# Kernel tuning notes

Measured on AMD Instinct MI355X. Metric: run time of the kernel, lower is better.

Reference implementation:

```python
import jax, jax.numpy as jnp
import numpy as np


def _reverse_padded(x, lengths):
    # x: [T, B, D]; reverse each sequence within its own length (packed-seq semantics)
    T = x.shape[0]
    t = jnp.arange(T)[:, None]                                   # [T, 1]
    idx = jnp.where(t < lengths[None, :], lengths[None, :] - 1 - t, t)  # [T, B]
    return jnp.take_along_axis(x, idx[:, :, None], axis=0)


def _lstm_dir(x, w_ih, w_hh, b):
    # single-direction LSTM, torch gate order (i, f, g, o). x: [T, B, Din]
    T, B, _ = x.shape
    H = w_hh.shape[1]
    xg = jnp.einsum('tbi,gi->tbg', x, w_ih) + b  # precompute input projections [T,B,4H]

    def step(carry, g_x):
        h, c = carry
        g = g_x + h @ w_hh.T
        i, f, gc, o = jnp.split(g, 4, axis=-1)
        c = jax.nn.sigmoid(f) * c + jax.nn.sigmoid(i) * jnp.tanh(gc)
        h = jax.nn.sigmoid(o) * jnp.tanh(c)
        return (h, c), h

    h0 = jnp.zeros((B, H), x.dtype)
    _, hs = jax.lax.scan(step, (h0, h0), xg)
    return hs  # [T, B, H]


def _bilstm_layer(x, lengths, wf, whf, bf, wr, whr, br):
    fwd = _lstm_dir(x, wf, whf, bf)
    rev = _reverse_padded(_lstm_dir(_reverse_padded(x, lengths), wr, whr, br), lengths)
    return jnp.concatenate([fwd, rev], axis=-1)  # [T, B, 2H]


def setup_inputs() -> dict:
    T, B, D, H = 256, 128, 300, 256
    key = jax.random.key(0)
    ks = jax.random.split(key, 24)
    stdv = 1.0 / np.sqrt(H)

    def u(k, shape):
        return jax.random.uniform(k, shape, jnp.float32, -stdv, stdv)

    inp = {
        'x': jax.random.normal(ks[0], (T, B, D), jnp.float32),
        'lengths': jax.random.randint(ks[1], (B,), 1, T + 1),
        # layer 0 forward / reverse
        'w_ih_l0': u(ks[2], (4 * H, D)), 'w_hh_l0': u(ks[3], (4 * H, H)),
        'b_ih_l0': u(ks[4], (4 * H,)), 'b_hh_l0': u(ks[5], (4 * H,)),
        'w_ih_l0r': u(ks[6], (4 * H, D)), 'w_hh_l0r': u(ks[7], (4 * H, H)),
        'b_ih_l0r': u(ks[8], (4 * H,)), 'b_hh_l0r': u(ks[9], (4 * H,)),
        # layer 1 forward / reverse (input dim 2H)
        'w_ih_l1': u(ks[10], (4 * H, 2 * H)), 'w_hh_l1': u(ks[11], (4 * H, H)),
        'b_ih_l1': u(ks[12], (4 * H,)), 'b_hh_l1': u(ks[13], (4 * H,)),
        'w_ih_l1r': u(ks[14], (4 * H, 2 * H)), 'w_hh_l1r': u(ks[15], (4 * H, H)),
        'b_ih_l1r': u(ks[16], (4 * H,)), 'b_hh_l1r': u(ks[17], (4 * H,)),
        # attention MLP + context vector
        'mlp_w': u(ks[18], (2 * H, 2 * H)),
        'mlp_b': u(ks[19], (2 * H,)),
        'ctx': jax.random.normal(ks[20], (2 * H,), jnp.float32) * 0.1,
    }
    return inp


def reference(x, lengths, w_ih_l0, w_hh_l0, b_ih_l0, b_hh_l0,
              w_ih_l0r, w_hh_l0r, b_ih_l0r, b_hh_l0r,
              w_ih_l1, w_hh_l1, b_ih_l1, b_hh_l1,
              w_ih_l1r, w_hh_l1r, b_ih_l1r, b_hh_l1r,
              mlp_w, mlp_b, ctx):
    lengths = jnp.maximum(lengths, 1)
    h1 = _bilstm_layer(x, lengths, w_ih_l0, w_hh_l0, b_ih_l0 + b_hh_l0,
                       w_ih_l0r, w_hh_l0r, b_ih_l0r + b_hh_l0r)
    h2 = _bilstm_layer(h1, lengths, w_ih_l1, w_hh_l1, b_ih_l1 + b_hh_l1,
                       w_ih_l1r, w_hh_l1r, b_ih_l1r + b_hh_l1r)
    out = h2.transpose(1, 0, 2)                                  # [B, T, 2H]
    ann = jnp.tanh(jnp.einsum('btd,ed->bte', out, mlp_w) + mlp_b)  # [B, T, 2H]
    scores = ann @ ctx                                           # [B, T]
    T = out.shape[1]
    mask = jnp.arange(T)[None, :] < lengths[:, None]             # [B, T]
    w = jax.nn.softmax(jnp.where(mask, scores, -1e9), axis=1)    # masked softmax over time
    return jnp.einsum('bt,btd->bd', w, out)                      # [B, 2H]
```

## Files before the change

kernel.cpp:

```cpp
#include <hip/hip_runtime.h>


#define T_ 256
#define B_ 128
#define D_ 300
#define H_ 256
#define G4H 1024
#define H2 512
#define TC 64
#define LDK 40
#define LDA 264

typedef __attribute__((ext_vector_type(8))) short bf16x8;
typedef __attribute__((ext_vector_type(4))) short short4v;
typedef __attribute__((ext_vector_type(4))) float f32x4;

#define MFMA16(a, b, c) __builtin_amdgcn_mfma_f32_16x16x32_bf16(a, b, c, 0, 0, 0)

__device__ __forceinline__ float sigf(float x) { return 1.f / (1.f + __expf(-x)); }
__device__ __forceinline__ float tanhfast(float x) { return 2.f / (1.f + __expf(-2.f * x)) - 1.f; }

__device__ __forceinline__ short hi_bf16(float x) {
  return (short)(__float_as_uint(x) >> 16);
}
__device__ __forceinline__ short lo_bf16(float x) {
  float lo = x - __uint_as_float(__float_as_uint(x) & 0xFFFF0000u);
  return (short)(__float_as_uint(lo) >> 16);
}

__device__ __forceinline__ void split_f4(const float4 v, short* hp, short* lp) {
  short4v h, l;
  h.x = hi_bf16(v.x); l.x = lo_bf16(v.x);
  h.y = hi_bf16(v.y); l.y = lo_bf16(v.y);
  h.z = hi_bf16(v.z); l.z = lo_bf16(v.z);
  h.w = hi_bf16(v.w); l.w = lo_bf16(v.w);
  *(short4v*)hp = h;
  *(short4v*)lp = l;
}

__device__ __forceinline__ void split8(const float4 v0, const float4 v1,
                                       bf16x8* hp, bf16x8* lp) {
  bf16x8 h, l;
  h[0] = hi_bf16(v0.x); l[0] = lo_bf16(v0.x);
  h[1] = hi_bf16(v0.y); l[1] = lo_bf16(v0.y);
  h[2] = hi_bf16(v0.z); l[2] = lo_bf16(v0.z);
  h[3] = hi_bf16(v0.w); l[3] = lo_bf16(v0.w);
  h[4] = hi_bf16(v1.x); l[4] = lo_bf16(v1.x);
  h[5] = hi_bf16(v1.y); l[5] = lo_bf16(v1.y);
  h[6] = hi_bf16(v1.z); l[6] = lo_bf16(v1.z);
  h[7] = hi_bf16(v1.w); l[7] = lo_bf16(v1.w);
  *hp = h; *lp = l;
}

__global__ __launch_bounds__(256, 2) void proj_gemm2(
    const float* __restrict__ X,
    const float* __restrict__ W0, const float* __restrict__ W1,
    const float* __restrict__ b1f, const float* __restrict__ b2f,
    const float* __restrict__ b1r, const float* __restrict__ b2r,
    float* __restrict__ C0, float* __restrict__ C1,
    int N, int K, const int* __restrict__ lengths, int t0)
{
  __shared__ short Xh[128 * LDK], Xl[128 * LDK];
  __shared__ short Wh[128 * LDK], Wl[128 * LDK];
  const int rev = blockIdx.z;
  const float* __restrict__ W = rev ? W1 : W0;
  const float* __restrict__ bias1 = rev ? b1r : b1f;
  const float* __restrict__ bias2 = rev ? b2r : b2f;
  float* __restrict__ C = rev ? C1 : C0;

  const int tid = threadIdx.x;
  const int m0 = blockIdx.y * 128, n0 = blockIdx.x * 128;
  const int s_step = t0 + blockIdx.y;

  const int sr = tid >> 3;
  const int sc = (tid & 7) * 4;
  const float* px[4];
  const float* pw[4];
#pragma unroll
  for (int p = 0; p < 4; p++) {
    const int r = sr + p * 32;
    int ss = s_step;
    if (rev) {
      int lb = lengths[r]; if (lb < 1) lb = 1;
      ss = (s_step < lb) ? (lb - 1 - s_step) : s_step;
    }
    px[p] = X + (size_t)(ss * 128 + r) * K;
    pw[p] = W + (size_t)(n0 + r) * K;
  }

  const int lane = tid & 63, w = tid >> 6;
  const int mb = (w & 1) * 64, nb = (w >> 1) * 64;
  const int r16 = lane & 15, quad = lane >> 4;

  f32x4 acc[4][4];
#pragma unroll
  for (int i = 0; i < 4; i++)
#pragma unroll
    for (int j = 0; j < 4; j++) acc[i][j] = (f32x4){0.f, 0.f, 0.f, 0.f};

  for (int k0 = 0; k0 < K; k0 += 32) {
    const int gk = k0 + sc;
    const bool kin = (gk < K);
#pragma unroll
    for (int p = 0; p < 4; p++) {
      float4 xv = {0.f, 0.f, 0.f, 0.f}, wv = {0.f, 0.f, 0.f, 0.f};
      if (kin) { xv = *(const float4*)(px[p] + gk); wv = *(const float4*)(pw[p] + gk); }
      const int ro = (sr + p * 32) * LDK + sc;
      split_f4(xv, &Xh[ro], &Xl[ro]);
      split_f4(wv, &Wh[ro], &Wl[ro]);
    }
    __syncthreads();

    bf16x8 ah[4], al[4], bh[4], bl[4];
#pragma unroll
    for (int mt = 0; mt < 4; mt++) {
      const int ro = (mb + mt * 16 + r16) * LDK + quad * 8;
      ah[mt] = *(const bf16x8*)&Xh[ro];
      al[mt] = *(const bf16x8*)&Xl[ro];
    }
#pragma unroll
    for (int nt = 0; nt < 4; nt++) {
      const int ro = (nb + nt * 16 + r16) * LDK + quad * 8;
      bh[nt] = *(const bf16x8*)&Wh[ro];
      bl[nt] = *(const bf16x8*)&Wl[ro];
    }
#pragma unroll
    for (int mt = 0; mt < 4; mt++)
#pragma unroll
      for (int nt = 0; nt < 4; nt++) {
        acc[mt][nt] = __builtin_amdgcn_mfma_f32_16x16x32_bf16(ah[mt], bh[nt], acc[mt][nt], 0, 0, 0);
        acc[mt][nt] = __builtin_amdgcn_mfma_f32_16x16x32_bf16(ah[mt], bl[nt], acc[mt][nt], 0, 0, 0);
        acc[mt][nt] = __builtin_amdgcn_mfma_f32_16x16x32_bf16(al[mt], bh[nt], acc[mt][nt], 0, 0, 0);
      }
    __syncthreads();
  }

  float bsum[4];
#pragma unroll
  for (int nt = 0; nt < 4; nt++) {
    const int col = n0 + nb + nt * 16 + r16;
    bsum[nt] = bias1[col] + bias2[col];
  }
#pragma unroll
  for (int mt = 0; mt < 4; mt++) {
    const int row = m0 + mb + mt * 16 + quad * 4;
#pragma unroll
    for (int nt = 0; nt < 4; nt++) {
      const int col = n0 + nb + nt * 16 + r16;
      float* Cp = C + (size_t)row * N + col;
#pragma unroll
      for (int reg = 0; reg < 4; reg++)
        Cp[(size_t)reg * N] = acc[mt][nt][reg] + bsum[nt];
    }
  }
}

__global__ __launch_bounds__(256, 2) void attn_gemm(
    const float* __restrict__ X, const float* __restrict__ W,
    const float* __restrict__ mlp_b, const float* __restrict__ ctx,
    float* __restrict__ scores, int M, int N, int K)
{
  __shared__ short Xh[128 * LDK], Xl[128 * LDK];
  __shared__ short Wh[128 * LDK], Wl[128 * LDK];
  const int tid = threadIdx.x;
  const int m0 = blockIdx.y * 128, n0 = blockIdx.x * 128;

  const int sr = tid >> 3;
  const int sc = (tid & 7) * 4;
  const float* px[4];
  const float* pw[4];
#pragma unroll
  for (int p = 0; p < 4; p++) {
    px[p] = X + (size_t)(m0 + sr + p * 32) * K;
    pw[p] = W + (size_t)(n0 + sr + p * 32) * K;
  }

  const int lane = tid & 63, w = tid >> 6;
  const int mb = (w & 1) * 64, nb = (w >> 1) * 64;
  const int r16 = lane & 15, quad = lane >> 4;

  f32x4 acc[4][4];
#pragma unroll
  for (int i = 0; i < 4; i++)
#pragma unroll
    for (int j = 0; j < 4; j++) acc[i][j] = (f32x4){0.f, 0.f, 0.f, 0.f};

  for (int k0 = 0; k0 < K; k0 += 32) {
    const int gk = k0 + sc;
#pragma unroll
    for (int p = 0; p < 4; p++) {
      float4 xv = *(const float4*)(px[p] + gk);
      float4 wv = *(const float4*)(pw[p] + gk);
      const int ro = (sr + p * 32) * LDK + sc;
      split_f4(xv, &Xh[ro], &Xl[ro]);
      split_f4(wv, &Wh[ro], &Wl[ro]);
    }
    __syncthreads();

    bf16x8 ah[4], al[4], bh[4], bl[4];
#pragma unroll
    for (int mt = 0; mt < 4; mt++) {
      const int ro = (mb + mt * 16 + r16) * LDK + quad * 8;
      ah[mt] = *(const bf16x8*)&Xh[ro];
      al[mt] = *(const bf16x8*)&Xl[ro];
    }
#pragma unroll
    for (int nt = 0; nt < 4; nt++) {
      const int ro = (nb + nt * 16 + r16) * LDK + quad * 8;
      bh[nt] = *(const bf16x8*)&Wh[ro];
      bl[nt] = *(const bf16x8*)&Wl[ro];
    }
#pragma unroll
    for (int mt = 0; mt < 4; mt++)
#pragma unroll
      for (int nt = 0; nt < 4; nt++) {
        acc[mt][nt] = __builtin_amdgcn_mfma_f32_16x16x32_bf16(ah[mt], bh[nt], acc[mt][nt], 0, 0, 0);
        acc[mt][nt] = __builtin_amdgcn_mfma_f32_16x16x32_bf16(ah[mt], bl[nt], acc[mt][nt], 0, 0, 0);
        acc[mt][nt] = __builtin_amdgcn_mfma_f32_16x16x32_bf16(al[mt], bh[nt], acc[mt][nt], 0, 0, 0);
      }
    __syncthreads();
  }

  float bb4[4], cc4[4];
#pragma unroll
  for (int nt = 0; nt < 4; nt++) {
    const int col = n0 + nb + nt * 16 + r16;
    bb4[nt] = mlp_b[col];
    cc4[nt] = ctx[col];
  }
#pragma unroll
  for (int mt = 0; mt < 4; mt++) {
#pragma unroll
    for (int reg = 0; reg < 4; reg++) {
      float ssum = 0.f;
#pragma unroll
      for (int nt = 0; nt < 4; nt++)
        ssum += tanhfast(acc[mt][nt][reg] + bb4[nt]) * cc4[nt];
      ssum += __shfl_xor(ssum, 1);
      ssum += __shfl_xor(ssum, 2);
      ssum += __shfl_xor(ssum, 4);
      ssum += __shfl_xor(ssum, 8);
      if (r16 == 0)
        atomicAdd(&scores[m0 + mb + mt * 16 + quad * 4 + reg], ssum);
    }
  }
}

__global__ __launch_bounds__(256, 1) void lstm_rec(
    const float* __restrict__ xgF, const float* __restrict__ xgR,
    const float* __restrict__ whF, const float* __restrict__ whR,
    const int* __restrict__ lengths, float* __restrict__ hout,
    float* __restrict__ ring, float* __restrict__ bbuf, float* __restrict__ cbuf,
    int t0)
{
  __shared__ short Ah[16 * LDA];
  __shared__ short Al[16 * LDA];
  __shared__ float gbuf[8 * 128];

  const int tid = threadIdx.x;
  const int blk = blockIdx.x;
  const int s = blk >> 5;
  const int d = (blk >> 4) & 1;
  const int g = blk & 15;
  const float* __restrict__ xg = d ? xgR : xgF;
  const float* __restrict__ wh = d ? whR : whF;

  const int lane = tid & 63;
  const int w = tid >> 6;
  const int r16 = lane & 15, quad = lane >> 4;

  const int cb = tid >> 5;
  const int hl = tid & 31;
  const int b = g * 8 + cb;
  const int hdim = s * 32 + hl;
  const int k0 = hl * 8;

  bf16x8 bh[2][8], bl[2][8];
#pragma unroll
  for (int nt = 0; nt < 2; nt++)
#pragma unroll
    for (int kt = 0; kt < 8; kt++) {
      const float* wr = wh + (size_t)(w * 256 + s * 32 + nt * 16 + r16) * 256
                           + kt * 32 + quad * 8;
      float4 v0 = *(const float4*)(wr);
      float4 v1 = *(const float4*)(wr + 4);
      split8(v0, v1, &bh[nt][kt], &bl[nt][kt]);
    }

  {
    int* za = (int*)(Ah + 8 * LDA);
    int* zb = (int*)(Al + 8 * LDA);
    for (int i = tid; i < (8 * LDA) / 2; i += 256) { za[i] = 0; zb[i] = 0; }
  }

  float c;
  if (t0 == 0) {
    int* za = (int*)Ah;
    int* zb = (int*)Al;
    for (int i = tid; i < (8 * LDA) / 2; i += 256) { za[i] = 0; zb[i] = 0; }
    c = 0.f;
  } else {
    const float* src = bbuf + ((size_t)d * 128 + g * 8 + cb) * 256 + k0;
    float4 v0 = *(const float4*)src;
    float4 v1 = *(const float4*)(src + 4);
    bf16x8 hv, lv;
    split8(v0, v1, &hv, &lv);
    *(bf16x8*)&Ah[cb * LDA + k0] = hv;
    *(bf16x8*)&Al[cb * LDA + k0] = lv;
    c = cbuf[((size_t)d * 128 + b) * 256 + hdim];
  }
  int lb = lengths[b]; if (lb < 1) lb = 1;

  const float* xr0 = xg + (size_t)b * 1024 + hdim;
  float x0 = xr0[0], x1 = xr0[256], x2 = xr0[512], x3 = xr0[768];
  __syncthreads();

  const int tend = t0 + TC;
  for (int t = t0; t < tend; t++) {
    const int slot = t - t0;
    const bool last = (t == tend - 1);

    f32x4 aH0 = {0.f,0.f,0.f,0.f}, aM0 = {0.f,0.f,0.f,0.f}, aL0 = {0.f,0.f,0.f,0.f};
    f32x4 aH1 = {0.f,0.f,0.f,0.f}, aM1 = {0.f,0.f,0.f,0.f}, aL1 = {0.f,0.f,0.f,0.f};
#pragma unroll
    for (int kt = 0; kt < 8; kt++) {
      const int ro = r16 * LDA + kt * 32 + quad * 8;
      bf16x8 ahf = *(const bf16x8*)&Ah[ro];
      bf16x8 alf = *(const bf16x8*)&Al[ro];
      aH0 = MFMA16(ahf, bh[0][kt], aH0);
      aM0 = MFMA16(ahf, bl[0][kt], aM0);
      aL0 = MFMA16(alf, bh[0][kt], aL0);
      aH1 = MFMA16(ahf, bh[1][kt], aH1);
      aM1 = MFMA16(ahf, bl[1][kt], aM1);
      aL1 = MFMA16(alf, bh[1][kt], aL1);
    }
    if (quad < 2) {
#pragma unroll
      for (int reg = 0; reg < 4; reg++) {
        gbuf[(quad * 4 + reg) * 128 + w * 32 + r16]      = aH0[reg] + aM0[reg] + aL0[reg];
        gbuf[(quad * 4 + reg) * 128 + w * 32 + 16 + r16] = aH1[reg] + aM1[reg] + aL1[reg];
      }
    }
    __syncthreads();

    const float gi = gbuf[cb * 128 +       hl] + x0;
    const float gf = gbuf[cb * 128 +  32 + hl] + x1;
    const float gg = gbuf[cb * 128 +  64 + hl] + x2;
    const float go = gbuf[cb * 128 +  96 + hl] + x3;
    const float si = sigf(gi), sf = sigf(gf);
    const float tg = tanhfast(gg), so = sigf(go);
    c = sf * c + si * tg;
    const float h = so * tanhfast(c);
    if (!last) {
      __hip_atomic_store(&ring[(((size_t)slot * 2 + d) * 128 + b) * 256 + hdim], h,
                         __ATOMIC_RELAXED, __HIP_MEMORY_SCOPE_AGENT);
    } else {
      bbuf[((size_t)d * 128 + b) * 256 + hdim] = h;
    }
    const int tin = d ? ((t < lb) ? (lb - 1 - t) : t) : t;
    hout[((size_t)tin * 128 + b) * 512 + d * 256 + hdim] = h;

    if (!last) {
      const float* xn = xg + ((size_t)(t + 1 - t0) * 128 + b) * 1024 + hdim;
      const float nx0 = xn[0], nx1 = xn[256], nx2 = xn[512], nx3 = xn[768];

      const unsigned* su = (const unsigned*)(ring +
          (((size_t)slot * 2 + d) * 128 + g * 8 + cb) * 256 + k0);
      unsigned uv[8];
      int it = 0;
      for (;;) {
        bool ok = true;
#pragma unroll
        for (int j = 0; j < 8; j++) {
          uv[j] = __hip_atomic_load(&su[j],
                                    __ATOMIC_RELAXED, __HIP_MEMORY_SCOPE_AGENT);
          ok &= (uv[j] != 0xFFFFFFFFu);
        }
        if (ok || ++it >= 20000) break;
      }
      float4 v0, v1;
      v0.x = __uint_as_float(uv[0]); v0.y = __uint_as_float(uv[1]);
      v0.z = __uint_as_float(uv[2]); v0.w = __uint_as_float(uv[3]);
      v1.x = __uint_as_float(uv[4]); v1.y = __uint_as_float(uv[5]);
      v1.z = __uint_as_float(uv[6]); v1.w = __uint_as_float(uv[7]);
      bf16x8 hv, lv;
      split8(v0, v1, &hv, &lv);
      *(bf16x8*)&Ah[cb * LDA + k0] = hv;
      *(bf16x8*)&Al[cb * LDA + k0] = lv;

      x0 = nx0; x1 = nx1; x2 = nx2; x3 = nx3;
      __syncthreads();
    }
  }
  cbuf[((size_t)d * 128 + b) * 256 + hdim] = c;
}

__global__ __launch_bounds__(256) void attn_final(
    const float* __restrict__ h2, const float* __restrict__ scores,
    const int* __restrict__ lengths, float* __restrict__ out)
{
  __shared__ float sl[256];
  __shared__ float red[256];
  const int b = blockIdx.x, tid = threadIdx.x;
  int lb = lengths[b]; if (lb < 1) lb = 1;
  const float sc = scores[(size_t)tid * 128 + b];
  const bool valid = (tid < lb);
  red[tid] = valid ? sc : -1e30f;
  __syncthreads();
  for (int off = 128; off > 0; off >>= 1) {
    if (tid < off) red[tid] = fmaxf(red[tid], red[tid + off]);
    __syncthreads();
  }
  const float mx = red[0];
  __syncthreads();
  const float p = valid ? __expf(sc - mx) : 0.f;
  red[tid] = p;
  __syncthreads();
  for (int off = 128; off > 0; off >>= 1) {
    if (tid < off) red[tid] += red[tid + off];
    __syncthreads();
  }
  const float inv = 1.f / red[0];
  __syncthreads();
  sl[tid] = p * inv;
  __syncthreads();

  float ax = 0.f, ay = 0.f;
  const int dd = tid * 2;
  for (int t = 0; t < 256; t++) {
    const float w = sl[t];
    if (w != 0.f) {
      const float* row = h2 + ((size_t)t * 128 + b) * 512 + dd;
      ax += w * row[0];
      ay += w * row[1];
    }
  }
  float2 r; r.x = ax; r.y = ay;
  *(float2*)(out + (size_t)b * 512 + dd) = r;
}

extern "C" void kernel_launch(void* const* d_in, const int* in_sizes, int n_in,
                              void* d_out, int out_size, void* d_ws, size_t ws_size,
                              hipStream_t stream) {
  (void)in_sizes; (void)n_in; (void)out_size; (void)ws_size;
  const float* x        = (const float*)d_in[0];
  const int*   lengths  = (const int*)d_in[1];
  const float* w_ih_l0  = (const float*)d_in[2];
  const float* w_hh_l0  = (const float*)d_in[3];
  const float* b_ih_l0  = (const float*)d_in[4];
  const float* b_hh_l0  = (const float*)d_in[5];
  const float* w_ih_l0r = (const float*)d_in[6];
  const float* w_hh_l0r = (const float*)d_in[7];
  const float* b_ih_l0r = (const float*)d_in[8];
  const float* b_hh_l0r = (const float*)d_in[9];
  const float* w_ih_l1  = (const float*)d_in[10];
  const float* w_hh_l1  = (const float*)d_in[11];
  const float* b_ih_l1  = (const float*)d_in[12];
  const float* b_hh_l1  = (const float*)d_in[13];
  const float* w_ih_l1r = (const float*)d_in[14];
  const float* w_hh_l1r = (const float*)d_in[15];
  const float* b_ih_l1r = (const float*)d_in[16];
  const float* b_hh_l1r = (const float*)d_in[17];
  const float* mlp_w    = (const float*)d_in[18];
  const float* mlp_b    = (const float*)d_in[19];
  const float* ctx      = (const float*)d_in[20];
  float* out = (float*)d_out;

  float* ws = (float*)d_ws;
  const size_t XGC    = (size_t)TC * B_ * G4H;
  const size_t H_SZ   = (size_t)T_ * B_ * H2;
  const size_t RINGSZ = (size_t)TC * 2 * B_ * H_;
  float* xgA    = ws;
  float* xgB    = xgA + XGC;
  float* h1     = xgB + XGC;
  float* h2     = h1 + H_SZ;
  float* ring   = h2 + H_SZ;
  float* bbuf   = ring + RINGSZ;
  float* cbuf   = bbuf + 65536;
  float* scores = cbuf + 65536;

  (void)hipMemsetAsync(scores, 0, 32768 * 4, stream);

  dim3 blk(256);
  const dim3 pgrid(G4H / 128, TC, 2);

  for (int c = 0; c < T_ / TC; c++) {
    const int t0 = c * TC;
    proj_gemm2<<<pgrid, blk, 0, stream>>>(x, w_ih_l0, w_ih_l0r,
                                          b_ih_l0, b_hh_l0, b_ih_l0r, b_hh_l0r,
                                          xgA, xgB, G4H, D_, lengths, t0);
    (void)hipMemsetAsync(ring, 0xFF, RINGSZ * 4, stream);
    lstm_rec<<<256, blk, 0, stream>>>(xgA, xgB, w_hh_l0, w_hh_l0r, lengths, h1,
                                      ring, bbuf, cbuf, t0);
  }
  for (int c = 0; c < T_ / TC; c++) {
    const int t0 = c * TC;
    proj_gemm2<<<pgrid, blk, 0, stream>>>(h1, w_ih_l1, w_ih_l1r,
                                          b_ih_l1, b_hh_l1, b_ih_l1r, b_hh_l1r,
                                          xgA, xgB, G4H, H2, lengths, t0);
    (void)hipMemsetAsync(ring, 0xFF, RINGSZ * 4, stream);
    lstm_rec<<<256, blk, 0, stream>>>(xgA, xgB, w_hh_l1, w_hh_l1r, lengths, h2,
                                      ring, bbuf, cbuf, t0);
  }
  attn_gemm<<<dim3(H2 / 128, (T_ * B_) / 128), blk, 0, stream>>>(h2, mlp_w, mlp_b, ctx, scores, T_ * B_, H2, H2);
  attn_final<<<B_, blk, 0, stream>>>(h2, scores, lengths, out);
}
```

Baseline: 2.385 ms.

## Process 32 batch rows per LSTM recurrence block and launch 64 blocks

The persistent recurrence kernel is regridded so each block handles 32 batch rows (two 16-row MFMA tiles) instead of 8, shrinking the grid from 256 to 64 blocks. Each block now does more MFMA work per step, but fewer blocks spin on the global ring buffer, and the same register-resident W_hh slices are reused across twice as many rows. The cost is fewer CUs in use and a longer serial critical path per timestep, since each block computes two tiles per step.

```diff
diff --git a/kernel.cpp b/kernel.cpp
--- a/kernel.cpp
+++ b/kernel.cpp
@@ -253,15 +253,16 @@
     float* __restrict__ ring, float* __restrict__ bbuf, float* __restrict__ cbuf,
     int t0)
 {
-  __shared__ short Ah[16 * LDA];
-  __shared__ short Al[16 * LDA];
-  __shared__ float gbuf[8 * 128];
+  __shared__ short Ah[2][16 * LDA];
+  __shared__ short Al[2][16 * LDA];
+  __shared__ float gbuf[2][16 * 128];
 
   const int tid = threadIdx.x;
   const int blk = blockIdx.x;
-  const int s = blk >> 5;
-  const int d = (blk >> 4) & 1;
-  const int g = blk & 15;
+  const int s = blk >> 3;
+  const int d = (blk >> 2) & 1;
+  const int p = blk & 3;
+  const int bbase = p * 32;
   const float* __restrict__ xg = d ? xgR : xgF;
   const float* __restrict__ wh = d ? whR : whF;
 
@@ -269,13 +270,13 @@
   const int w = tid >> 6;
   const int r16 = lane & 15, quad = lane >> 4;
 
-  const int cb = tid >> 5;
+  const int rb = tid >> 4;
+  const int kc = (tid & 15) * 16;
+  const int q = tid >> 5;
   const int hl = tid & 31;
-  const int b = g * 8 + cb;
   const int hdim = s * 32 + hl;
-  const int k0 = hl * 8;
-
-  bf16x8 bh[2][8], bl[2][8];
+
+  bf16x8 wbh[2][8], wbl[2][8];
 #pragma unroll
   for (int nt = 0; nt < 2; nt++)
 #pragma unroll
@@ -284,35 +285,52 @@
                            + kt * 32 + quad * 8;
       float4 v0 = *(const float4*)(wr);
       float4 v1 = *(const float4*)(wr + 4);
-      split8(v0, v1, &bh[nt][kt], &bl[nt][kt]);
-    }
-
-  {
-    int* za = (int*)(Ah + 8 * LDA);
-    int* zb = (int*)(Al + 8 * LDA);
-    for (int i = tid; i < (8 * LDA) / 2; i += 256) { za[i] = 0; zb[i] = 0; }
-  }
-
-  float c;
+      split8(v0, v1, &wbh[nt][kt], &wbl[nt][kt]);
+    }
+
+  float cc[2][2];
+  int   lbv[2][2];
+  float xreg[2][2][4];
+#pragma unroll
+  for (int u = 0; u < 2; u++)
+#pragma unroll
+    for (int hf = 0; hf < 2; hf++) {
+      const int b = bbase + u * 16 + hf * 8 + q;
+      int lb = lengths[b]; if (lb < 1) lb = 1;
+      lbv[u][hf] = lb;
+      const float* xr = xg + (size_t)b * 1024 + hdim;
+      xreg[u][hf][0] = xr[0];   xreg[u][hf][1] = xr[256];
+      xreg[u][hf][2] = xr[512]; xreg[u][hf][3] = xr[768];
+    }
+
   if (t0 == 0) {
-    int* za = (int*)Ah;
-    int* zb = (int*)Al;
-    for (int i = tid; i < (8 * LDA) / 2; i += 256) { za[i] = 0; zb[i] = 0; }
-    c = 0.f;
+    int* za = (int*)&Ah[0][0];
+    int* zb = (int*)&Al[0][0];
+    for (int i = tid; i < (2 * 16 * LDA) / 2; i += 256) { za[i] = 0; zb[i] = 0; }
+#pragma unroll
+    for (int u = 0; u < 2; u++)
+#pragma unroll
+      for (int hf = 0; hf < 2; hf++) cc[u][hf] = 0.f;
   } else {
-    const float* src = bbuf + ((size_t)d * 128 + g * 8 + cb) * 256 + k0;
-    float4 v0 = *(const float4*)src;
-    float4 v1 = *(const float4*)(src + 4);
-    bf16x8 hv, lv;
-    split8(v0, v1, &hv, &lv);
-    *(bf16x8*)&Ah[cb * LDA + k0] = hv;
-    *(bf16x8*)&Al[cb * LDA + k0] = lv;
-    c = cbuf[((size_t)d * 128 + b) * 256 + hdim];
-  }
-  int lb = lengths[b]; if (lb < 1) lb = 1;
-
-  const float* xr0 = xg + (size_t)b * 1024 + hdim;
-  float x0 = xr0[0], x1 = xr0[256], x2 = xr0[512], x3 = xr0[768];
+#pragma unroll
+    for (int u = 0; u < 2; u++) {
+      const float* src = bbuf + ((size_t)d * 128 + bbase + u * 16 + rb) * 256 + kc;
+      float4 v0 = *(const float4*)(src);
+      float4 v1 = *(const float4*)(src + 4);
+      float4 v2 = *(const float4*)(src + 8);
+      float4 v3 = *(const float4*)(src + 12);
+      bf16x8 hv, lv;
+      split8(v0, v1, &hv, &lv);
+      *(bf16x8*)&Ah[u][rb * LDA + kc] = hv;
+      *(bf16x8*)&Al[u][rb * LDA + kc] = lv;
+      split8(v2, v3, &hv, &lv);
+      *(bf16x8*)&Ah[u][rb * LDA + kc + 8] = hv;
+      *(bf16x8*)&Al[u][rb * LDA + kc + 8] = lv;
+#pragma unroll
+      for (int hf = 0; hf < 2; hf++)
+        cc[u][hf] = cbuf[((size_t)d * 128 + bbase + u * 16 + hf * 8 + q) * 256 + hdim];
+    }
+  }
   __syncthreads();
 
   const int tend = t0 + TC;
@@ -320,79 +338,108 @@
     const int slot = t - t0;
     const bool last = (t == tend - 1);
 
-    f32x4 aH0 = {0.f,0.f,0.f,0.f}, aM0 = {0.f,0.f,0.f,0.f}, aL0 = {0.f,0.f,0.f,0.f};
-    f32x4 aH1 = {0.f,0.f,0.f,0.f}, aM1 = {0.f,0.f,0.f,0.f}, aL1 = {0.f,0.f,0.f,0.f};
-#pragma unroll
-    for (int kt = 0; kt < 8; kt++) {
-      const int ro = r16 * LDA + kt * 32 + quad * 8;
-      bf16x8 ahf = *(const bf16x8*)&Ah[ro];
-      bf16x8 alf = *(const bf16x8*)&Al[ro];
-      aH0 = MFMA16(ahf, bh[0][kt], aH0);
-      aM0 = MFMA16(ahf, bl[0][kt], aM0);
-      aL0 = MFMA16(alf, bh[0][kt], aL0);
-      aH1 = MFMA16(ahf, bh[1][kt], aH1);
-      aM1 = MFMA16(ahf, bl[1][kt], aM1);
-      aL1 = MFMA16(alf, bh[1][kt], aL1);
-    }
-    if (quad < 2) {
+#pragma unroll
+    for (int u = 0; u < 2; u++) {
+      f32x4 aH0 = {0.f,0.f,0.f,0.f}, aM0 = {0.f,0.f,0.f,0.f}, aL0 = {0.f,0.f,0.f,0.f};
+      f32x4 aH1 = {0.f,0.f,0.f,0.f}, aM1 = {0.f,0.f,0.f,0.f}, aL1 = {0.f,0.f,0.f,0.f};
+#pragma unroll
+      for (int kt = 0; kt < 8; kt++) {
+        const int ro = r16 * LDA + kt * 32 + quad * 8;
+        bf16x8 ahf = *(const bf16x8*)&Ah[u][ro];
+        bf16x8 alf = *(const bf16x8*)&Al[u][ro];
+        aH0 = MFMA16(ahf, wbh[0][kt], aH0);
+        aM0 = MFMA16(ahf, wbl[0][kt], aM0);
+        aL0 = MFMA16(alf, wbh[0][kt], aL0);
+        aH1 = MFMA16(ahf, wbh[1][kt], aH1);
+        aM1 = MFMA16(ahf, wbl[1][kt], aM1);
+        aL1 = MFMA16(alf, wbh[1][kt], aL1);
+      }
 #pragma unroll
       for (int reg = 0; reg < 4; reg++) {
-        gbuf[(quad * 4 + reg) * 128 + w * 32 + r16]      = aH0[reg] + aM0[reg] + aL0[reg];
-        gbuf[(quad * 4 + reg) * 128 + w * 32 + 16 + r16] = aH1[reg] + aM1[reg] + aL1[reg];
+        gbuf[u][(quad * 4 + reg) * 128 + w * 32 + r16]      = aH0[reg] + aM0[reg] + aL0[reg];
+        gbuf[u][(quad * 4 + reg) * 128 + w * 32 + 16 + r16] = aH1[reg] + aM1[reg] + aL1[reg];
       }
     }
     __syncthreads();
 
-    const float gi = gbuf[cb * 128 +       hl] + x0;
-    const float gf = gbuf[cb * 128 +  32 + hl] + x1;
-    const float gg = gbuf[cb * 128 +  64 + hl] + x2;
-    const float go = gbuf[cb * 128 +  96 + hl] + x3;
-    const float si = sigf(gi), sf = sigf(gf);
-    const float tg = tanhfast(gg), so = sigf(go);
-    c = sf * c + si * tg;
-    const float h = so * tanhfast(c);
+#pragma unroll
+    for (int u = 0; u < 2; u++)
+#pragma unroll
+      for (int hf = 0; hf < 2; hf++) {
+        const int rbq = hf * 8 + q;
+        const int b = bbase + u * 16 + rbq;
+        const float gi = gbuf[u][rbq * 128 +       hl] + xreg[u][hf][0];
+        const float gf = gbuf[u][rbq * 128 +  32 + hl] + xreg[u][hf][1];
+        const float gg = gbuf[u][rbq * 128 +  64 + hl] + xreg[u][hf][2];
+        const float go = gbuf[u][rbq * 128 +  96 + hl] + xreg[u][hf][3];
+        const float si = sigf(gi), sf = sigf(gf);
+        const float tg = tanhfast(gg), so = sigf(go);
+        float c = sf * cc[u][hf] + si * tg;
+        cc[u][hf] = c;
+        const float h = so * tanhfast(c);
+        if (!last) {
+          __hip_atomic_store(&ring[(((size_t)slot * 2 + d) * 128 + b) * 256 + hdim], h,
+                             __ATOMIC_RELAXED, __HIP_MEMORY_SCOPE_AGENT);
+        } else {
+          bbuf[((size_t)d * 128 + b) * 256 + hdim] = h;
+        }
+        const int lb = lbv[u][hf];
+        const int tin = d ? ((t < lb) ? (lb - 1 - t) : t) : t;
+        hout[((size_t)tin * 128 + b) * 512 + d * 256 + hdim] = h;
+      }
+
     if (!last) {
-      __hip_atomic_store(&ring[(((size_t)slot * 2 + d) * 128 + b) * 256 + hdim], h,
-                         __ATOMIC_RELAXED, __HIP_MEMORY_SCOPE_AGENT);
-    } else {
-      bbuf[((size_t)d * 128 + b) * 256 + hdim] = h;
-    }
-    const int tin = d ? ((t < lb) ? (lb - 1 - t) : t) : t;
-    hout[((size_t)tin * 128 + b) * 512 + d * 256 + hdim] = h;
-
-    if (!last) {
-      const float* xn = xg + ((size_t)(t + 1 - t0) * 128 + b) * 1024 + hdim;
-      const float nx0 = xn[0], nx1 = xn[256], nx2 = xn[512], nx3 = xn[768];
-
-      const unsigned* su = (const unsigned*)(ring +
-          (((size_t)slot * 2 + d) * 128 + g * 8 + cb) * 256 + k0);
-      unsigned uv[8];
-      int it = 0;
-      for (;;) {
-        bool ok = true;
-#pragma unroll
-        for (int j = 0; j < 8; j++) {
-          uv[j] = __hip_atomic_load(&su[j],
-                                    __ATOMIC_RELAXED, __HIP_MEMORY_SCOPE_AGENT);
-          ok &= (uv[j] != 0xFFFFFFFFu);
+#pragma unroll
+      for (int u = 0; u < 2; u++)
+#pragma unroll
+        for (int hf = 0; hf < 2; hf++) {
+          const int b = bbase + u * 16 + hf * 8 + q;
+          const float* xn = xg + ((size_t)(t + 1 - t0) * 128 + b) * 1024 + hdim;
+          xreg[u][hf][0] = xn[0];   xreg[u][hf][1] = xn[256];
+          xreg[u][hf][2] = xn[512]; xreg[u][hf][3] = xn[768];
         }
-        if (ok || ++it >= 20000) break;
+
+#pragma unroll
+      for (int u = 0; u < 2; u++) {
+        const unsigned* su = (const unsigned*)(ring +
+            (((size_t)slot * 2 + d) * 128 + bbase + u * 16 + rb) * 256 + kc);
+        unsigned uv[16];
+        int it = 0;
+        for (;;) {
+          bool ok = true;
+#pragma unroll
+          for (int j = 0; j < 16; j++) {
+            uv[j] = __hip_atomic_load(&su[j],
+                                      __ATOMIC_RELAXED, __HIP_MEMORY_SCOPE_AGENT);
+            ok &= (uv[j] != 0xFFFFFFFFu);
+          }
+          if (ok || ++it >= 20000) break;
+        }
+        float4 v0, v1;
+        bf16x8 hv, lv;
+        v0.x = __uint_as_float(uv[0]);  v0.y = __uint_as_float(uv[1]);
+        v0.z = __uint_as_float(uv[2]);  v0.w = __uint_as_float(uv[3]);
+        v1.x = __uint_as_float(uv[4]);  v1.y = __uint_as_float(uv[5]);
+        v1.z = __uint_as_float(uv[6]);  v1.w = __uint_as_float(uv[7]);
+        split8(v0, v1, &hv, &lv);
+        *(bf16x8*)&Ah[u][rb * LDA + kc] = hv;
+        *(bf16x8*)&Al[u][rb * LDA + kc] = lv;
+        v0.x = __uint_as_float(uv[8]);  v0.y = __uint_as_float(uv[9]);
+        v0.z = __uint_as_float(uv[10]); v0.w = __uint_as_float(uv[11]);
+        v1.x = __uint_as_float(uv[12]); v1.y = __uint_as_float(uv[13]);
+        v1.z = __uint_as_float(uv[14]); v1.w = __uint_as_float(uv[15]);
+        split8(v0, v1, &hv, &lv);
+        *(bf16x8*)&Ah[u][rb * LDA + kc + 8] = hv;
+        *(bf16x8*)&Al[u][rb * LDA + kc + 8] = lv;
       }
-      float4 v0, v1;
-      v0.x = __uint_as_float(uv[0]); v0.y = __uint_as_float(uv[1]);
-      v0.z = __uint_as_float(uv[2]); v0.w = __uint_as_float(uv[3]);
-      v1.x = __uint_as_float(uv[4]); v1.y = __uint_as_float(uv[5]);
-      v1.z = __uint_as_float(uv[6]); v1.w = __uint_as_float(uv[7]);
-      bf16x8 hv, lv;
-      split8(v0, v1, &hv, &lv);
-      *(bf16x8*)&Ah[cb * LDA + k0] = hv;
-      *(bf16x8*)&Al[cb * LDA + k0] = lv;
-
-      x0 = nx0; x1 = nx1; x2 = nx2; x3 = nx3;
       __syncthreads();
     }
   }
-  cbuf[((size_t)d * 128 + b) * 256 + hdim] = c;
+#pragma unroll
+  for (int u = 0; u < 2; u++)
+#pragma unroll
+    for (int hf = 0; hf < 2; hf++)
+      cbuf[((size_t)d * 128 + bbase + u * 16 + hf * 8 + q) * 256 + hdim] = cc[u][hf];
 }
 
 __global__ __launch_bounds__(256) void attn_final(
@@ -490,8 +537,8 @@
                                           b_ih_l0, b_hh_l0, b_ih_l0r, b_hh_l0r,
                                           xgA, xgB, G4H, D_, lengths, t0);
     (void)hipMemsetAsync(ring, 0xFF, RINGSZ * 4, stream);
-    lstm_rec<<<256, blk, 0, stream>>>(xgA, xgB, w_hh_l0, w_hh_l0r, lengths, h1,
-                                      ring, bbuf, cbuf, t0);
+    lstm_rec<<<64, blk, 0, stream>>>(xgA, xgB, w_hh_l0, w_hh_l0r, lengths, h1,
+                                     ring, bbuf, cbuf, t0);
   }
   for (int c = 0; c < T_ / TC; c++) {
     const int t0 = c * TC;
@@ -499,8 +546,8 @@
                                           b_ih_l1, b_hh_l1, b_ih_l1r, b_hh_l1r,
                                           xgA, xgB, G4H, H2, lengths, t0);
     (void)hipMemsetAsync(ring, 0xFF, RINGSZ * 4, stream);
-    lstm_rec<<<256, blk, 0, stream>>>(xgA, xgB, w_hh_l1, w_hh_l1r, lengths, h2,
-                                      ring, bbuf, cbuf, t0);
+    lstm_rec<<<64, blk, 0, stream>>>(xgA, xgB, w_hh_l1, w_hh_l1r, lengths, h2,
+                                     ring, bbuf, cbuf, t0);
   }
   attn_gemm<<<dim3(H2 / 128, (T_ * B_) / 128), blk, 0, stream>>>(h2, mlp_w, mlp_b, ctx, scores, T_ * B_, H2, H2);
   attn_final<<<B_, blk, 0, stream>>>(h2, scores, lengths, out);
```

Measured after the change: 4.114 ms. 72.4% more time.

## Interleave both LSTM directions per block with 16-row batch tiles and bf16 ring exchange

Applied to the files above, without the earlier changes.

The recurrent kernel drops from 256 to 64 blocks. Each block now holds weights for both directions and processes 16 batch rows instead of 8, so the full 16-row MFMA tile is used rather than half of it being zero padding. The two directions alternate inside each time step, so one direction's spin-wait on the cross-block ring can overlap the other's compute. The ring now carries pre-split bf16 hi/lo halves packed in 32-bit words, which removes the split work on the consumer side. In exchange, register pressure roughly doubles from holding two weight sets, and each block has more work per step on the serial chain.

```diff
diff --git a/kernel.cpp b/kernel.cpp
--- a/kernel.cpp
+++ b/kernel.cpp
@@ -16,6 +16,8 @@
 typedef __attribute__((ext_vector_type(4))) float f32x4;
 
 #define MFMA16(a, b, c) __builtin_amdgcn_mfma_f32_16x16x32_bf16(a, b, c, 0, 0, 0)
+#define ATOM_ST(p, v) __hip_atomic_store((p), (v), __ATOMIC_RELAXED, __HIP_MEMORY_SCOPE_AGENT)
+#define ATOM_LD(p) __hip_atomic_load((p), __ATOMIC_RELAXED, __HIP_MEMORY_SCOPE_AGENT)
 
 __device__ __forceinline__ float sigf(float x) { return 1.f / (1.f + __expf(-x)); }
 __device__ __forceinline__ float tanhfast(float x) { return 2.f / (1.f + __expf(-2.f * x)) - 1.f; }
@@ -253,146 +255,184 @@
     float* __restrict__ ring, float* __restrict__ bbuf, float* __restrict__ cbuf,
     int t0)
 {
-  __shared__ short Ah[16 * LDA];
-  __shared__ short Al[16 * LDA];
-  __shared__ float gbuf[8 * 128];
+  __shared__ short Ah[2][16 * LDA];
+  __shared__ short Al[2][16 * LDA];
+  __shared__ float gbuf[16 * 128];
 
   const int tid = threadIdx.x;
   const int blk = blockIdx.x;
-  const int s = blk >> 5;
-  const int d = (blk >> 4) & 1;
-  const int g = blk & 15;
-  const float* __restrict__ xg = d ? xgR : xgF;
-  const float* __restrict__ wh = d ? whR : whF;
+  const int s = blk >> 3;
+  const int g = blk & 7;
+  const int bbase = g * 16;
+  unsigned* __restrict__ ring32 = (unsigned*)ring;
 
   const int lane = tid & 63;
   const int w = tid >> 6;
   const int r16 = lane & 15, quad = lane >> 4;
 
-  const int cb = tid >> 5;
-  const int hl = tid & 31;
-  const int b = g * 8 + cb;
-  const int hdim = s * 32 + hl;
-  const int k0 = hl * 8;
-
-  bf16x8 bh[2][8], bl[2][8];
-#pragma unroll
-  for (int nt = 0; nt < 2; nt++)
+  const int b = tid >> 4;
+  const int hlp = tid & 15;
+  const int hl0 = hlp * 2;
+  const int bg = bbase + b;
+  const int hdim0 = s * 32 + hl0;
+
+  bf16x8 wbh[2][2][8], wbl[2][2][8];
+#pragma unroll
+  for (int dd = 0; dd < 2; dd++) {
+    const float* whd = dd ? whR : whF;
+#pragma unroll
+    for (int nt = 0; nt < 2; nt++)
+#pragma unroll
+      for (int kt = 0; kt < 8; kt++) {
+        const float* wr = whd + (size_t)(w * 256 + s * 32 + nt * 16 + r16) * 256
+                              + kt * 32 + quad * 8;
+        float4 v0 = *(const float4*)(wr);
+        float4 v1 = *(const float4*)(wr + 4);
+        split8(v0, v1, &wbh[dd][nt][kt], &wbl[dd][nt][kt]);
+      }
+  }
+
+  int lb = lengths[bg]; if (lb < 1) lb = 1;
+
+  float2 xr[2][4];
+#pragma unroll
+  for (int dd = 0; dd < 2; dd++) {
+    const float* xgd = dd ? xgR : xgF;
+#pragma unroll
+    for (int gate = 0; gate < 4; gate++)
+      xr[dd][gate] = *(const float2*)(xgd + (size_t)bg * 1024 + gate * 256 + hdim0);
+  }
+
+  float cc[2][2];
+  if (t0 == 0) {
+    int* za = (int*)&Ah[0][0];
+    int* zb = (int*)&Al[0][0];
+    for (int i = tid; i < (2 * 16 * LDA) / 2; i += 256) { za[i] = 0; zb[i] = 0; }
+    cc[0][0] = cc[0][1] = cc[1][0] = cc[1][1] = 0.f;
+  } else {
+    const int b2 = tid >> 4, k0 = (tid & 15) * 16;
+#pragma unroll
+    for (int dd = 0; dd < 2; dd++) {
+      const float* src = bbuf + ((size_t)dd * 128 + bbase + b2) * 256 + k0;
+      float4 v0 = *(const float4*)(src);
+      float4 v1 = *(const float4*)(src + 4);
+      float4 v2 = *(const float4*)(src + 8);
+      float4 v3 = *(const float4*)(src + 12);
+      bf16x8 hv, lv;
+      split8(v0, v1, &hv, &lv);
+      *(bf16x8*)&Ah[dd][b2 * LDA + k0] = hv;
+      *(bf16x8*)&Al[dd][b2 * LDA + k0] = lv;
+      split8(v2, v3, &hv, &lv);
+      *(bf16x8*)&Ah[dd][b2 * LDA + k0 + 8] = hv;
+      *(bf16x8*)&Al[dd][b2 * LDA + k0 + 8] = lv;
+      const float2 cv = *(const float2*)(cbuf + ((size_t)dd * 128 + bg) * 256 + hdim0);
+      cc[dd][0] = cv.x; cc[dd][1] = cv.y;
+    }
+  }
+  __syncthreads();
+
+  auto chain_phase = [&](int dd, int t) {
+    const int slot = t - t0;
+    const bool last = (t == t0 + TC - 1);
+
+    f32x4 aH0 = {0.f,0.f,0.f,0.f}, aM0 = {0.f,0.f,0.f,0.f}, aL0 = {0.f,0.f,0.f,0.f};
+    f32x4 aH1 = {0.f,0.f,0.f,0.f}, aM1 = {0.f,0.f,0.f,0.f}, aL1 = {0.f,0.f,0.f,0.f};
 #pragma unroll
     for (int kt = 0; kt < 8; kt++) {
-      const float* wr = wh + (size_t)(w * 256 + s * 32 + nt * 16 + r16) * 256
-                           + kt * 32 + quad * 8;
-      float4 v0 = *(const float4*)(wr);
-      float4 v1 = *(const float4*)(wr + 4);
-      split8(v0, v1, &bh[nt][kt], &bl[nt][kt]);
-    }
-
-  {
-    int* za = (int*)(Ah + 8 * LDA);
-    int* zb = (int*)(Al + 8 * LDA);
-    for (int i = tid; i < (8 * LDA) / 2; i += 256) { za[i] = 0; zb[i] = 0; }
-  }
-
-  float c;
-  if (t0 == 0) {
-    int* za = (int*)Ah;
-    int* zb = (int*)Al;
-    for (int i = tid; i < (8 * LDA) / 2; i += 256) { za[i] = 0; zb[i] = 0; }
-    c = 0.f;
-  } else {
-    const float* src = bbuf + ((size_t)d * 128 + g * 8 + cb) * 256 + k0;
-    float4 v0 = *(const float4*)src;
-    float4 v1 = *(const float4*)(src + 4);
-    bf16x8 hv, lv;
-    split8(v0, v1, &hv, &lv);
-    *(bf16x8*)&Ah[cb * LDA + k0] = hv;
-    *(bf16x8*)&Al[cb * LDA + k0] = lv;
-    c = cbuf[((size_t)d * 128 + b) * 256 + hdim];
-  }
-  int lb = lengths[b]; if (lb < 1) lb = 1;
-
-  const float* xr0 = xg + (size_t)b * 1024 + hdim;
-  float x0 = xr0[0], x1 = xr0[256], x2 = xr0[512], x3 = xr0[768];
-  __syncthreads();
+      const int ro = r16 * LDA + kt * 32 + quad * 8;
+      bf16x8 ahf = *(const bf16x8*)&Ah[dd][ro];
+      bf16x8 alf = *(const bf16x8*)&Al[dd][ro];
+      aH0 = MFMA16(ahf, wbh[dd][0][kt], aH0);
+      aM0 = MFMA16(ahf, wbl[dd][0][kt], aM0);
+      aL0 = MFMA16(alf, wbh[dd][0][kt], aL0);
+      aH1 = MFMA16(ahf, wbh[dd][1][kt], aH1);
+      aM1 = MFMA16(ahf, wbl[dd][1][kt], aM1);
+      aL1 = MFMA16(alf, wbh[dd][1][kt], aL1);
+    }
+#pragma unroll
+    for (int reg = 0; reg < 4; reg++) {
+      gbuf[(quad * 4 + reg) * 128 + w * 32 + r16]      = aH0[reg] + aM0[reg] + aL0[reg];
+      gbuf[(quad * 4 + reg) * 128 + w * 32 + 16 + r16] = aH1[reg] + aM1[reg] + aL1[reg];
+    }
+    __syncthreads();
+
+    const float2 g0 = *(const float2*)&gbuf[b * 128 +       hl0];
+    const float2 g1 = *(const float2*)&gbuf[b * 128 +  32 + hl0];
+    const float2 g2 = *(const float2*)&gbuf[b * 128 +  64 + hl0];
+    const float2 g3 = *(const float2*)&gbuf[b * 128 +  96 + hl0];
+
+    const float si0 = sigf(g0.x + xr[dd][0].x), si1 = sigf(g0.y + xr[dd][0].y);
+    const float sf0 = sigf(g1.x + xr[dd][1].x), sf1 = sigf(g1.y + xr[dd][1].y);
+    const float tg0 = tanhfast(g2.x + xr[dd][2].x), tg1 = tanhfast(g2.y + xr[dd][2].y);
+    const float so0 = sigf(g3.x + xr[dd][3].x), so1 = sigf(g3.y + xr[dd][3].y);
+    const float c0 = sf0 * cc[dd][0] + si0 * tg0;
+    const float c1 = sf1 * cc[dd][1] + si1 * tg1;
+    cc[dd][0] = c0; cc[dd][1] = c1;
+    const float h0 = so0 * tanhfast(c0);
+    const float h1 = so1 * tanhfast(c1);
+
+    if (!last) {
+      const unsigned ph = (unsigned)(unsigned short)hi_bf16(h0)
+                        | ((unsigned)(unsigned short)hi_bf16(h1) << 16);
+      const unsigned pl = (unsigned)(unsigned short)lo_bf16(h0)
+                        | ((unsigned)(unsigned short)lo_bf16(h1) << 16);
+      unsigned* rp = ring32 + (((size_t)slot * 2 + dd) * 8 + g) * 4096 + s * 256 + tid;
+      ATOM_ST(rp, ph);
+      ATOM_ST(rp + 2048, pl);
+    } else {
+      float2 hv; hv.x = h0; hv.y = h1;
+      *(float2*)(bbuf + ((size_t)dd * 128 + bg) * 256 + hdim0) = hv;
+    }
+    const int tin = dd ? ((t < lb) ? (lb - 1 - t) : t) : t;
+    float2 hv2; hv2.x = h0; hv2.y = h1;
+    *(float2*)(hout + ((size_t)tin * 128 + bg) * 512 + dd * 256 + hdim0) = hv2;
+
+    if (!last) {
+      const float* xgd = dd ? xgR : xgF;
+#pragma unroll
+      for (int gate = 0; gate < 4; gate++)
+        xr[dd][gate] = *(const float2*)(xgd +
+            ((size_t)(slot + 1) * 128 + bg) * 1024 + gate * 256 + hdim0);
+    }
+  };
+
+  auto spin_stage = [&](int dd, int slotm1) {
+    const unsigned* su = ring32 + (((size_t)slotm1 * 2 + dd) * 8 + g) * 4096;
+    unsigned uv[16];
+    int it = 0;
+    for (;;) {
+      bool ok = true;
+#pragma unroll
+      for (int j = 0; j < 16; j++) {
+        uv[j] = ATOM_LD(&su[j * 256 + tid]);
+        ok &= (uv[j] != 0xFFFFFFFFu);
+      }
+      if (ok || ++it >= 20000) break;
+    }
+#pragma unroll
+    for (int j = 0; j < 16; j++) {
+      const int sp = j & 7;
+      const int off = (tid >> 4) * LDA + sp * 32 + (tid & 15) * 2;
+      if (j < 8) *(unsigned*)&Ah[dd][off] = uv[j];
+      else       *(unsigned*)&Al[dd][off] = uv[j];
+    }
+  };
 
   const int tend = t0 + TC;
   for (int t = t0; t < tend; t++) {
-    const int slot = t - t0;
-    const bool last = (t == tend - 1);
-
-    f32x4 aH0 = {0.f,0.f,0.f,0.f}, aM0 = {0.f,0.f,0.f,0.f}, aL0 = {0.f,0.f,0.f,0.f};
-    f32x4 aH1 = {0.f,0.f,0.f,0.f}, aM1 = {0.f,0.f,0.f,0.f}, aL1 = {0.f,0.f,0.f,0.f};
-#pragma unroll
-    for (int kt = 0; kt < 8; kt++) {
-      const int ro = r16 * LDA + kt * 32 + quad * 8;
-      bf16x8 ahf = *(const bf16x8*)&Ah[ro];
-      bf16x8 alf = *(const bf16x8*)&Al[ro];
-      aH0 = MFMA16(ahf, bh[0][kt], aH0);
-      aM0 = MFMA16(ahf, bl[0][kt], aM0);
-      aL0 = MFMA16(alf, bh[0][kt], aL0);
-      aH1 = MFMA16(ahf, bh[1][kt], aH1);
-      aM1 = MFMA16(ahf, bl[1][kt], aM1);
-      aL1 = MFMA16(alf, bh[1][kt], aL1);
-    }
-    if (quad < 2) {
-#pragma unroll
-      for (int reg = 0; reg < 4; reg++) {
-        gbuf[(quad * 4 + reg) * 128 + w * 32 + r16]      = aH0[reg] + aM0[reg] + aL0[reg];
-        gbuf[(quad * 4 + reg) * 128 + w * 32 + 16 + r16] = aH1[reg] + aM1[reg] + aL1[reg];
-      }
-    }
-    __syncthreads();
-
-    const float gi = gbuf[cb * 128 +       hl] + x0;
-    const float gf = gbuf[cb * 128 +  32 + hl] + x1;
-    const float gg = gbuf[cb * 128 +  64 + hl] + x2;
-    const float go = gbuf[cb * 128 +  96 + hl] + x3;
-    const float si = sigf(gi), sf = sigf(gf);
-    const float tg = tanhfast(gg), so = sigf(go);
-    c = sf * c + si * tg;
-    const float h = so * tanhfast(c);
-    if (!last) {
-      __hip_atomic_store(&ring[(((size_t)slot * 2 + d) * 128 + b) * 256 + hdim], h,
-                         __ATOMIC_RELAXED, __HIP_MEMORY_SCOPE_AGENT);
-    } else {
-      bbuf[((size_t)d * 128 + b) * 256 + hdim] = h;
-    }
-    const int tin = d ? ((t < lb) ? (lb - 1 - t) : t) : t;
-    hout[((size_t)tin * 128 + b) * 512 + d * 256 + hdim] = h;
-
-    if (!last) {
-      const float* xn = xg + ((size_t)(t + 1 - t0) * 128 + b) * 1024 + hdim;
-      const float nx0 = xn[0], nx1 = xn[256], nx2 = xn[512], nx3 = xn[768];
-
-      const unsigned* su = (const unsigned*)(ring +
-          (((size_t)slot * 2 + d) * 128 + g * 8 + cb) * 256 + k0);
-      unsigned uv[8];
-      int it = 0;
-      for (;;) {
-        bool ok = true;
-#pragma unroll
-        for (int j = 0; j < 8; j++) {
-          uv[j] = __hip_atomic_load(&su[j],
-                                    __ATOMIC_RELAXED, __HIP_MEMORY_SCOPE_AGENT);
-          ok &= (uv[j] != 0xFFFFFFFFu);
-        }
-        if (ok || ++it >= 20000) break;
-      }
-      float4 v0, v1;
-      v0.x = __uint_as_float(uv[0]); v0.y = __uint_as_float(uv[1]);
-      v0.z = __uint_as_float(uv[2]); v0.w = __uint_as_float(uv[3]);
-      v1.x = __uint_as_float(uv[4]); v1.y = __uint_as_float(uv[5]);
-      v1.z = __uint_as_float(uv[6]); v1.w = __uint_as_float(uv[7]);
-      bf16x8 hv, lv;
-      split8(v0, v1, &hv, &lv);
-      *(bf16x8*)&Ah[cb * LDA + k0] = hv;
-      *(bf16x8*)&Al[cb * LDA + k0] = lv;
-
-      x0 = nx0; x1 = nx1; x2 = nx2; x3 = nx3;
-      __syncthreads();
-    }
-  }
-  cbuf[((size_t)d * 128 + b) * 256 + hdim] = c;
+    if (t > t0) spin_stage(0, t - 1 - t0);
+    __syncthreads();
+    chain_phase(0, t);
+    if (t > t0) spin_stage(1, t - 1 - t0);
+    __syncthreads();
+    chain_phase(1, t);
+  }
+
+#pragma unroll
+  for (int dd = 0; dd < 2; dd++) {
+    float2 cv; cv.x = cc[dd][0]; cv.y = cc[dd][1];
+    *(float2*)(cbuf + ((size_t)dd * 128 + bg) * 256 + hdim0) = cv;
+  }
 }
 
 __global__ __launch_bounds__(256) void attn_final(
@@ -490,8 +530,8 @@
                                           b_ih_l0, b_hh_l0, b_ih_l0r, b_hh_l0r,
                                           xgA, xgB, G4H, D_, lengths, t0);
     (void)hipMemsetAsync(ring, 0xFF, RINGSZ * 4, stream);
-    lstm_rec<<<256, blk, 0, stream>>>(xgA, xgB, w_hh_l0, w_hh_l0r, lengths, h1,
-                                      ring, bbuf, cbuf, t0);
+    lstm_rec<<<64, blk, 0, stream>>>(xgA, xgB, w_hh_l0, w_hh_l0r, lengths, h1,
+                                     ring, bbuf, cbuf, t0);
   }
   for (int c = 0; c < T_ / TC; c++) {
     const int t0 = c * TC;
@@ -499,8 +539,8 @@
                                           b_ih_l1, b_hh_l1, b_ih_l1r, b_hh_l1r,
                                           xgA, xgB, G4H, H2, lengths, t0);
     (void)hipMemsetAsync(ring, 0xFF, RINGSZ * 4, stream);
-    lstm_rec<<<256, blk, 0, stream>>>(xgA, xgB, w_hh_l1, w_hh_l1r, lengths, h2,
-                                      ring, bbuf, cbuf, t0);
+    lstm_rec<<<64, blk, 0, stream>>>(xgA, xgB, w_hh_l1, w_hh_l1r, lengths, h2,
+                                     ring, bbuf, cbuf, t0);
   }
   attn_gemm<<<dim3(H2 / 128, (T_ * B_) / 128), blk, 0, stream>>>(h2, mlp_w, mlp_b, ctx, scores, T_ * B_, H2, H2);
   attn_final<<<B_, blk, 0, stream>>>(h2, scores, lengths, out);
```

Result: slower. 2.987 ms (+25.2%).
